# Kernel optimization log

Hardware: AMD Instinct MI355X
Metric: run time of the kernel (lower is better)

## Reference

```python
import jax, jax.numpy as jnp
import numpy as np

B, L, D_MODEL = 8, 2048, 768
D_INNER, D_STATE, DT_RANK, K = 1536, 16, 48, 4


def setup_inputs() -> dict:
    key = jax.random.key(0)
    ks = jax.random.split(key, 9)
    s = 0.02
    return {
        "hidden_states": jax.random.normal(ks[0], (B, L, D_MODEL), jnp.float32),
        "W_in": jax.random.normal(ks[1], (D_MODEL, 2 * D_INNER), jnp.float32) * s,
        "conv_w": jax.random.normal(ks[2], (D_INNER, 1, K), jnp.float32) * s,
        "conv_b": jax.random.normal(ks[3], (D_INNER,), jnp.float32) * s,
        "W_x": jax.random.normal(ks[4], (DT_RANK + 2 * D_STATE, D_INNER), jnp.float32) * s,
        "W_dt": jax.random.normal(ks[5], (D_INNER, DT_RANK), jnp.float32) * s,
        "b_dt": jax.random.normal(ks[6], (D_INNER,), jnp.float32) * s,
        "A_log": jax.random.normal(ks[7], (D_INNER, D_STATE), jnp.float32),
        "D_param": jax.random.normal(ks[8], (D_INNER,), jnp.float32),
    }


def _mamba(hidden_states, W_in, conv_w, conv_b, W_x, W_dt, b_dt, A_log, D_param):
    # in_proj then chunk into ssm branch (x) and gating residual (res)
    xz = hidden_states @ W_in                      # (B, L, 2*d_inner)
    x, res = jnp.split(xz, 2, axis=-1)             # each (B, L, d_inner)

    # causal depthwise conv over time, then SiLU
    xc = x.transpose(0, 2, 1)                      # (B, C, L)
    xc = jax.lax.conv_general_dilated(
        xc, conv_w, window_strides=(1,), padding=[(K - 1, 0)],
        feature_group_count=D_INNER, dimension_numbers=("NCH", "OIH", "NCH"))
    x = jax.nn.silu(xc + conv_b[None, :, None]).transpose(0, 2, 1)  # (B, L, d_inner)

    # input-dependent SSM parameters
    x_dbl = x @ W_x.T                              # (B, L, dt_rank + 2*d_state)
    dt = jax.nn.softplus(x_dbl[..., :DT_RANK] @ W_dt.T + b_dt)      # (B, L, d_inner)
    Bm = x_dbl[..., DT_RANK:DT_RANK + D_STATE]     # (B, L, d_state)
    Cm = x_dbl[..., DT_RANK + D_STATE:]            # (B, L, d_state)
    A = -jnp.exp(A_log)                            # (d_inner, d_state)

    def step(h, inp):
        x_t, dt_t, B_t, C_t = inp                  # (B,d_inner),(B,d_inner),(B,d_state),(B,d_state)
        dA = jnp.exp(dt_t[..., None] * A)          # (B, d_inner, d_state)
        dBx = (dt_t * x_t)[..., None] * B_t[:, None, :]
        h = dA * h + dBx
        y = jnp.einsum("bds,bs->bd", h, C_t)
        return h, y

    xs = (x.transpose(1, 0, 2), dt.transpose(1, 0, 2),
          Bm.transpose(1, 0, 2), Cm.transpose(1, 0, 2))
    h0 = jnp.zeros((x.shape[0], D_INNER, D_STATE), x.dtype)
    _, ys = jax.lax.scan(step, h0, xs)             # ys: (L, B, d_inner)
    y = ys.transpose(1, 0, 2) + x * D_param        # skip term
    return y * jax.nn.silu(res)                    # gated output (B, L, d_inner)


def reference(hidden_states, W_in, conv_w, conv_b, W_x, W_dt, b_dt, A_log, D_param):
    return _mamba(hidden_states, W_in, conv_w, conv_b, W_x, W_dt, b_dt, A_log, D_param)
```

## Files before the change

### kernel.cpp

```cpp
#include <hip/hip_runtime.h>
#include <hip/hip_bf16.h>
#include <stdint.h>

#define B_SZ 8
#define L_SZ 2048
#define DM 768
#define DI 1536
#define DS 16
#define DR 48
#define M_SZ (B_SZ * L_SZ)
#define N1 (2 * DI)

#define NC 64
#define TC (L_SZ / NC)
#define CH (B_SZ * DI)
#define KS 2
#define NT2 (DM / 32)
#define L2E 1.44269504088896f

typedef short short8 __attribute__((ext_vector_type(8)));
typedef float f32x4 __attribute__((ext_vector_type(4)));
typedef float f32x2 __attribute__((ext_vector_type(2)));

__device__ __forceinline__ ushort f2b(float f) {
  __hip_bfloat16 h = __float2bfloat16(f);
  return *reinterpret_cast<ushort*>(&h);
}
__device__ __forceinline__ float b2f(ushort u) {
  __hip_bfloat16 h;
  *reinterpret_cast<ushort*>(&h) = u;
  return __bfloat162float(h);
}
__device__ __forceinline__ ushort f2h(float f) {
  _Float16 h = (_Float16)f;
  return *reinterpret_cast<ushort*>(&h);
}
__device__ __forceinline__ float h2f(ushort u) {
  _Float16 h;
  *reinterpret_cast<ushort*>(&h) = u;
  return (float)h;
}

__device__ __forceinline__ void gl16(const ushort* g, ushort* l) {
  __builtin_amdgcn_global_load_lds(
      (const __attribute__((address_space(1))) void*)g,
      (__attribute__((address_space(3))) void*)l, 16, 0, 0);
}


__global__ __launch_bounds__(256) void prep_all(const float4* __restrict__ hs4,
                                                const float* __restrict__ w_in,
                                                const float* __restrict__ wx_f,
                                                const float* __restrict__ wdt_f,
                                                ushort4* __restrict__ A1,
                                                ushort* __restrict__ wt,
                                                ushort* __restrict__ wx_b,
                                                ushort* __restrict__ wdt_p) {
  const int n4 = M_SZ * DM / 4;
  const int nT = 3072 * 96;
  const int nwx = 80 * DI;
  const int nwdt = DI * 64;
  int idx = blockIdx.x * 256 + threadIdx.x;
  if (idx < n4) {
    float4 v = hs4[idx];
    ushort4 o;
    o.x = f2b(v.x); o.y = f2b(v.y); o.z = f2b(v.z); o.w = f2b(v.w);
    A1[idx] = o;
  } else if (idx < n4 + nT) {
    int j = idx - n4;
    int n = j % 3072;
    int kb = (j / 3072) * 8;
    short8 o;
#pragma unroll
    for (int q = 0; q < 8; ++q) o[q] = (short)f2b(w_in[(size_t)(kb + q) * 3072 + n]);
    *(short8*)(wt + (size_t)n * DM + kb) = o;
  } else if (idx < n4 + nT + nwx) {
    int j = idx - n4 - nT;
    wx_b[j] = f2b(wx_f[j]);
  } else if (idx < n4 + nT + nwx + nwdt) {
    int j = idx - n4 - nT - nwx;
    int col = j >> 6, k = j & 63;
    wdt_p[j] = (k < DR) ? f2b(wdt_f[col * DR + k]) : (ushort)0;
  }
}


__global__ __launch_bounds__(512, 1) void gemm_xz(const ushort* __restrict__ A,
                                                  const ushort* __restrict__ Bt,
                                                  ushort* __restrict__ xout,
                                                  ushort* __restrict__ gateout) {
  __shared__ ushort lds[49152];

  const int t = threadIdx.x;
  const int lane = t & 63;
  const int wid = t >> 6;
  const int wm = wid >> 2, wn = wid & 3;
  const int r = lane & 15, hi = lane >> 4;

  const int g = blockIdx.x;
  const int xcd = g & 7;
  const int local = g >> 3;
  const int bx = xcd * 8 + local / 12;
  const int by = local % 12;
  const int bm = bx * 256;
  const int bn = by * 256;

  const ushort* gsrc[4];
  int ldso[4];
#pragma unroll
  for (int i = 0; i < 4; ++i) {
    int c = wid * 4 + i;
    if (c < 16)
      gsrc[i] = A + (size_t)(bm + c * 16 + r) * DM + hi * 8;
    else
      gsrc[i] = Bt + (size_t)(bn + (c - 16) * 16 + r) * DM + hi * 8;
    ldso[i] = c * 512;
  }

  f32x4 acc[8][4];
#pragma unroll
  for (int m = 0; m < 8; ++m)
#pragma unroll
    for (int n = 0; n < 4; ++n) acc[m][n] = f32x4{0.f, 0.f, 0.f, 0.f};

  ushort* b0 = lds;
  ushort* b1 = lds + 16384;
  ushort* b2 = lds + 32768;

#pragma unroll
  for (int i = 0; i < 4; ++i) gl16(gsrc[i], b0 + ldso[i]);
#pragma unroll
  for (int i = 0; i < 4; ++i) gl16(gsrc[i] + 32, b1 + ldso[i]);
  asm volatile("s_waitcnt vmcnt(4)" ::: "memory");
  __builtin_amdgcn_s_barrier();

  for (int kt = 0; kt < NT2; ++kt) {
    const bool stage = (kt + 2 < NT2);
    const int koff = (kt + 2) * 32;

    short8 bfr[4];
#pragma unroll
    for (int n = 0; n < 4; ++n)
      bfr[n] = *(const short8*)&b0[(16 + wn * 4 + n) * 512 + lane * 8];

#pragma unroll
    for (int q = 0; q < 2; ++q) {
      short8 afr[4];
#pragma unroll
      for (int m = 0; m < 4; ++m)
        afr[m] = *(const short8*)&b0[(wm * 8 + q * 4 + m) * 512 + lane * 8];

      if (stage) {
        gl16(gsrc[2 * q] + koff, b2 + ldso[2 * q]);
        gl16(gsrc[2 * q + 1] + koff, b2 + ldso[2 * q + 1]);
      }

      asm volatile("s_barrier" ::: "memory");

      __builtin_amdgcn_s_setprio(1);
#pragma unroll
      for (int m = 0; m < 4; ++m)
#pragma unroll
        for (int n = 0; n < 4; ++n)
          acc[q * 4 + m][n] =
              __builtin_amdgcn_mfma_f32_16x16x32_bf16(afr[m], bfr[n], acc[q * 4 + m][n], 0, 0, 0);
      __builtin_amdgcn_s_setprio(0);

      if (q == 1) {
        if (stage)
          asm volatile("s_waitcnt vmcnt(4)" ::: "memory");
        else
          asm volatile("s_waitcnt vmcnt(0)" ::: "memory");
      }
      asm volatile("s_barrier" ::: "memory");
    }

    ushort* tmp = b0; b0 = b1; b1 = b2; b2 = tmp;
  }

  const bool isx = (bn < DI);
  ushort* outp = isx ? xout : gateout;
  const int cbase = bn - (isx ? 0 : DI) + wn * 64;
#pragma unroll
  for (int mf = 0; mf < 8; ++mf)
#pragma unroll
    for (int nf = 0; nf < 4; ++nf) {
      int col = cbase + nf * 16 + r;
#pragma unroll
      for (int j = 0; j < 4; ++j) {
        int row = bm + wm * 128 + mf * 16 + hi * 4 + j;
        float v = acc[mf][nf][j];
        if (!isx) v = v / (1.f + __expf(-v));
        outp[(size_t)row * DI + col] = f2b(v);
      }
    }
}


__global__ __launch_bounds__(256) void xdbl_conv(const ushort* __restrict__ xp,
                                                 const float* __restrict__ cw,
                                                 const float* __restrict__ cb,
                                                 const ushort* __restrict__ wx,
                                                 ushort* __restrict__ xc,
                                                 float* __restrict__ xdp) {
  __shared__ ushort Af[32 * 544];

  const int tid = threadIdx.x;
  const int row0 = blockIdx.x * 64;
  const int ks = blockIdx.y;

  const int lane = tid & 63, wid = tid >> 6;
  const int r = lane & 15, hi = lane >> 4;
  const int row0w = row0 + wid * 16;

  f32x4 acc[5];
#pragma unroll
  for (int n = 0; n < 5; ++n) acc[n] = f32x4{0.f, 0.f, 0.f, 0.f};

  const int rg = tid >> 5;
  const int c8 = tid & 31;
  const int col_loc = c8 * 8;
  const int chunkc = col_loc >> 5;
  const int hi_w = (col_loc & 31) >> 3;

  for (int sl = 0; sl < 3; ++sl) {
    const int kbeg = ks * 768 + sl * 256;
    if (sl) __syncthreads();

    {
      const int col = kbeg + col_loc;
      float4 cwv[8];
      float cbv[8];
#pragma unroll
      for (int e = 0; e < 8; ++e) {
        cwv[e] = *(const float4*)(cw + (size_t)(col + e) * 4);
        cbv[e] = cb[col + e];
      }
      short8 z8 = {0, 0, 0, 0, 0, 0, 0, 0};
#pragma unroll
      for (int j = 0; j < 8; ++j) {
        int row = row0 + rg * 8 + j;
        int l = row & (L_SZ - 1);
        const ushort* base = xp + (size_t)row * DI + col;
        short8 x0 = *(const short8*)base;
        short8 xm1 = (l >= 1) ? *(const short8*)(base - DI) : z8;
        short8 xm2 = (l >= 2) ? *(const short8*)(base - 2 * DI) : z8;
        short8 xm3 = (l >= 3) ? *(const short8*)(base - 3 * DI) : z8;
        short8 o;
#pragma unroll
        for (int e = 0; e < 8; ++e) {
          float4 w = cwv[e];
          float a = cbv[e] + w.x * b2f((ushort)xm3[e]) + w.y * b2f((ushort)xm2[e]) +
                    w.z * b2f((ushort)xm1[e]) + w.w * b2f((ushort)x0[e]);
          o[e] = (short)f2b(a / (1.f + __expf(-a)));
        }
        *(short8*)(xc + (size_t)row * DI + col) = o;
        int row_loc = rg * 8 + j;
        int chunk = (row_loc >> 4) * 8 + chunkc;
        int lane_t = (hi_w << 4) | (row_loc & 15);
        int slot = lane_t ^ (chunk & 7);
        *(short8*)&Af[chunk * 544 + slot * 8] = o;
      }
    }
    __syncthreads();

#pragma unroll
    for (int k0 = 0; k0 < 8; ++k0) {
      int chunk = wid * 8 + k0;
      short8 a = *(const short8*)&Af[chunk * 544 + ((lane ^ (chunk & 7)) * 8)];
      const int kk = kbeg + k0 * 32;
#pragma unroll
      for (int n = 0; n < 5; ++n) {
        short8 b = *(const short8*)(wx + (size_t)(n * 16 + r) * DI + kk + hi * 8);
        acc[n] = __builtin_amdgcn_mfma_f32_16x16x32_bf16(a, b, acc[n], 0, 0, 0);
      }
    }
  }

  float* op = xdp + (size_t)ks * M_SZ * 80;
#pragma unroll
  for (int n = 0; n < 5; ++n)
#pragma unroll
    for (int j = 0; j < 4; ++j)
      op[(size_t)(row0w + hi * 4 + j) * 80 + n * 16 + r] = acc[n][j];
}


__device__ __forceinline__ short8 pack8f(const float* p) {
  short8 v;
#pragma unroll
  for (int i = 0; i < 8; ++i) v[i] = (short)f2b(p[i]);
  return v;
}

__global__ __launch_bounds__(256) void dt_gemm(const float* __restrict__ xdp,
                                               const ushort* __restrict__ wdtp,
                                               const float* __restrict__ bdt,
                                               ushort* __restrict__ dt) {
  int wave = blockIdx.x * 4 + (threadIdx.x >> 6);
  int lane = threadIdx.x & 63;
  int r = lane & 15, hi = lane >> 4;
  int row0 = wave * 16;

  const float* p0 = xdp + (size_t)(row0 + r) * 80 + hi * 8;
  const float* p1 = p0 + (size_t)M_SZ * 80;

  float atmp[8];
  float4 q0 = *(const float4*)p0, q1 = *(const float4*)(p0 + 4);
  float4 s0 = *(const float4*)p1, s1 = *(const float4*)(p1 + 4);
  atmp[0] = q0.x + s0.x; atmp[1] = q0.y + s0.y; atmp[2] = q0.z + s0.z; atmp[3] = q0.w + s0.w;
  atmp[4] = q1.x + s1.x; atmp[5] = q1.y + s1.y; atmp[6] = q1.z + s1.z; atmp[7] = q1.w + s1.w;
  short8 a0 = pack8f(atmp);
  short8 a1 = {0, 0, 0, 0, 0, 0, 0, 0};
  if (hi < 2) {
    const float* p0b = p0 + 32 - hi * 8 + hi * 8;
    const float* q0p = xdp + (size_t)(row0 + r) * 80 + 32 + hi * 8;
    const float* q1p = q0p + (size_t)M_SZ * 80;
    float4 u0 = *(const float4*)q0p, u1 = *(const float4*)(q0p + 4);
    float4 v0 = *(const float4*)q1p, v1 = *(const float4*)(q1p + 4);
    atmp[0] = u0.x + v0.x; atmp[1] = u0.y + v0.y; atmp[2] = u0.z + v0.z; atmp[3] = u0.w + v0.w;
    atmp[4] = u1.x + v1.x; atmp[5] = u1.y + v1.y; atmp[6] = u1.z + v1.z; atmp[7] = u1.w + v1.w;
    a1 = pack8f(atmp);
    (void)p0b;
  }

  for (int nb = blockIdx.y * 6; nb < blockIdx.y * 6 + 6; ++nb) {
    int c0 = nb * 64;
    f32x4 acc[4];
#pragma unroll
    for (int n = 0; n < 4; ++n) acc[n] = f32x4{0.f, 0.f, 0.f, 0.f};
#pragma unroll
    for (int n = 0; n < 4; ++n) {
      const ushort* wp = wdtp + (size_t)(c0 + n * 16 + r) * 64;
      short8 b0 = *(const short8*)(wp + hi * 8);
      short8 b1 = *(const short8*)(wp + 32 + hi * 8);
      acc[n] = __builtin_amdgcn_mfma_f32_16x16x32_bf16(a0, b0, acc[n], 0, 0, 0);
      acc[n] = __builtin_amdgcn_mfma_f32_16x16x32_bf16(a1, b1, acc[n], 0, 0, 0);
    }
#pragma unroll
    for (int n = 0; n < 4; ++n)
#pragma unroll
      for (int j = 0; j < 4; ++j) {
        int col = c0 + n * 16 + r;
        float z = acc[n][j] + bdt[col];
        float sp = (z > 20.f) ? z : __logf(1.f + __expf(z));
        dt[(size_t)(row0 + hi * 4 + j) * DI + col] = f2h(sp);
      }
  }
}


__global__ __launch_bounds__(256) void scan_pass1(const ushort* __restrict__ dt,
                                                  const ushort* __restrict__ xc,
                                                  const float* __restrict__ xdp,
                                                  const float* __restrict__ A_log,
                                                  float* __restrict__ hend,
                                                  float* __restrict__ sumdt) {
  const int d = blockIdx.x * 256 + threadIdx.x;
  const int c = blockIdx.y, b = blockIdx.z;
  const int t0 = c * TC;

  __shared__ float Bs[TC * 16];
  for (int i = threadIdx.x; i < TC * 16; i += 256) {
    int tt = i >> 4, s = i & 15;
    size_t row = ((size_t)(b * L_SZ + t0 + tt)) * 80 + DR + s;
    Bs[i] = xdp[row] + xdp[(size_t)M_SZ * 80 + row];
  }

  f32x2 a2[8];
  const float4* al4 = (const float4*)(A_log + (size_t)d * DS);
#pragma unroll
  for (int q = 0; q < 4; ++q) {
    float4 v = al4[q];
    a2[2 * q] = f32x2{-__expf(v.x) * L2E, -__expf(v.y) * L2E};
    a2[2 * q + 1] = f32x2{-__expf(v.z) * L2E, -__expf(v.w) * L2E};
  }

  __syncthreads();

  f32x2 h2[8];
#pragma unroll
  for (int q = 0; q < 8; ++q) h2[q] = f32x2{0.f, 0.f};
  float sd = 0.f;

  const ushort* dtp = dt + ((size_t)b * L_SZ + t0) * DI + d;
  const ushort* xp = xc + ((size_t)b * L_SZ + t0) * DI + d;

  ushort dt0 = dtp[0], dt1 = dtp[DI];
  ushort xu0 = xp[0], xu1 = xp[DI];
  dtp += 2 * (size_t)DI; xp += 2 * (size_t)DI;
  const f32x4* bp4 = (const f32x4*)Bs;
#pragma unroll 2
  for (int tt = 0; tt < TC; ++tt) {
    ushort dtu = dt0, xu = xu0;
    dt0 = dt1; xu0 = xu1;
    dt1 = *dtp; xu1 = *xp;
    dtp += DI; xp += DI;
    float dtv = h2f(dtu);
    float xv = b2f(xu);
    sd += dtv;
    float dx = dtv * xv;
    f32x2 dts = f32x2{dtv, dtv};
    f32x2 dxs = f32x2{dx, dx};
#pragma unroll
    for (int q4 = 0; q4 < 4; ++q4) {
      f32x4 bq = bp4[q4];
#pragma unroll
      for (int hq = 0; hq < 2; ++hq) {
        int q = q4 * 2 + hq;
        f32x2 bv = f32x2{bq[2 * hq], bq[2 * hq + 1]};
        f32x2 arg, t2;
        asm("v_pk_mul_f32 %0, %1, %2" : "=v"(arg) : "v"(dts), "v"(a2[q]));
        float e0, e1;
        asm("v_exp_f32 %0, %1" : "=v"(e0) : "v"(arg[0]));
        asm("v_exp_f32 %0, %1" : "=v"(e1) : "v"(arg[1]));
        asm("v_pk_mul_f32 %0, %1, %2" : "=v"(t2) : "v"(dxs), "v"(bv));
        h2[q][0] = __builtin_fmaf(e0, h2[q][0], t2[0]);
        h2[q][1] = __builtin_fmaf(e1, h2[q][1], t2[1]);
      }
    }
    bp4 += 4;
  }

  const size_t ch = (size_t)b * DI + d;
  sumdt[ch * NC + c] = sd;
  f32x2* hp = (f32x2*)&hend[((size_t)c * CH + ch) * 16];
#pragma unroll
  for (int q = 0; q < 8; ++q) hp[q] = h2[q];
}


__global__ __launch_bounds__(256) void scan_pass2(const float* __restrict__ A_log,
                                                  const float* __restrict__ sumdt,
                                                  float* __restrict__ hbuf) {
  int idx = blockIdx.x * 256 + threadIdx.x;
  int ch = idx >> 4, s = idx & 15;
  int d = ch % DI;
  float A = -__expf(A_log[d * DS + s]);
  float h = 0.f;
  for (int c = 0; c < NC; ++c) {
    float* p = &hbuf[((size_t)c * CH + ch) * 16 + s];
    float he = *p;
    *p = h;
    float sd = sumdt[(size_t)ch * NC + c];
    h = __expf(A * sd) * h + he;
  }
}

__global__ __launch_bounds__(256) void scan_pass3(const ushort* __restrict__ dt,
                                                  const ushort* __restrict__ xc,
                                                  const float* __restrict__ xdp,
                                                  const ushort* __restrict__ gateb,
                                                  const float* __restrict__ A_log,
                                                  const float* __restrict__ Dp,
                                                  const float* __restrict__ hstart,
                                                  float* __restrict__ out) {
  const int d = blockIdx.x * 256 + threadIdx.x;
  const int c = blockIdx.y, b = blockIdx.z;
  const int t0 = c * TC;

  __shared__ float Bs[TC * 16];
  __shared__ float Cs[TC * 16];
  for (int i = threadIdx.x; i < TC * 16; i += 256) {
    int tt = i >> 4, s = i & 15;
    size_t row = ((size_t)(b * L_SZ + t0 + tt)) * 80;
    Bs[i] = xdp[row + DR + s] + xdp[(size_t)M_SZ * 80 + row + DR + s];
    Cs[i] = xdp[row + DR + DS + s] + xdp[(size_t)M_SZ * 80 + row + DR + DS + s];
  }

  f32x2 a2[8];
  const float4* al4 = (const float4*)(A_log + (size_t)d * DS);
#pragma unroll
  for (int q = 0; q < 4; ++q) {
    float4 v = al4[q];
    a2[2 * q] = f32x2{-__expf(v.x) * L2E, -__expf(v.y) * L2E};
    a2[2 * q + 1] = f32x2{-__expf(v.z) * L2E, -__expf(v.w) * L2E};
  }
  const float Dpv = Dp[d];

  const size_t ch = (size_t)b * DI + d;
  f32x2 h2[8];
  const f32x2* hp = (const f32x2*)&hstart[((size_t)c * CH + ch) * 16];
#pragma unroll
  for (int q = 0; q < 8; ++q) h2[q] = hp[q];

  __syncthreads();

  const ushort* dtp = dt + ((size_t)b * L_SZ + t0) * DI + d;
  const ushort* xp = xc + ((size_t)b * L_SZ + t0) * DI + d;
  const ushort* gp = gateb + ((size_t)b * L_SZ + t0) * DI + d;
  float* op = out + ((size_t)b * L_SZ + t0) * DI + d;

  ushort dt0 = dtp[0], dt1 = dtp[DI];
  ushort xu0 = xp[0], xu1 = xp[DI];
  ushort gu0 = gp[0], gu1 = gp[DI];
  dtp += 2 * (size_t)DI; xp += 2 * (size_t)DI; gp += 2 * (size_t)DI;
  const f32x4* bp4 = (const f32x4*)Bs;
  const f32x4* cp4 = (const f32x4*)Cs;
#pragma unroll 2
  for (int tt = 0; tt < TC; ++tt) {
    ushort dtu = dt0, xu = xu0, gu = gu0;
    dt0 = dt1; xu0 = xu1; gu0 = gu1;
    dt1 = *dtp; xu1 = *xp; gu1 = *gp;
    dtp += DI; xp += DI; gp += DI;
    float dtv = h2f(dtu);
    float xv = b2f(xu);
    float gv = b2f(gu);
    float dx = dtv * xv;
    f32x2 dts = f32x2{dtv, dtv};
    f32x2 dxs = f32x2{dx, dx};
    f32x2 ya = f32x2{0.f, 0.f}, yb = f32x2{0.f, 0.f};
#pragma unroll
    for (int q4 = 0; q4 < 4; ++q4) {
      f32x4 bq = bp4[q4];
      f32x4 cq = cp4[q4];
#pragma unroll
      for (int hq = 0; hq < 2; ++hq) {
        int q = q4 * 2 + hq;
        f32x2 bv = f32x2{bq[2 * hq], bq[2 * hq + 1]};
        f32x2 cv = f32x2{cq[2 * hq], cq[2 * hq + 1]};
        f32x2 arg, t2;
        asm("v_pk_mul_f32 %0, %1, %2" : "=v"(arg) : "v"(dts), "v"(a2[q]));
        float e0, e1;
        asm("v_exp_f32 %0, %1" : "=v"(e0) : "v"(arg[0]));
        asm("v_exp_f32 %0, %1" : "=v"(e1) : "v"(arg[1]));
        asm("v_pk_mul_f32 %0, %1, %2" : "=v"(t2) : "v"(dxs), "v"(bv));
        h2[q][0] = __builtin_fmaf(e0, h2[q][0], t2[0]);
        h2[q][1] = __builtin_fmaf(e1, h2[q][1], t2[1]);
        if (hq)
          asm("v_pk_fma_f32 %0, %1, %2, %0" : "+v"(yb) : "v"(h2[q]), "v"(cv));
        else
          asm("v_pk_fma_f32 %0, %1, %2, %0" : "+v"(ya) : "v"(h2[q]), "v"(cv));
      }
    }
    bp4 += 4; cp4 += 4;
    float y = (ya[0] + ya[1]) + (yb[0] + yb[1]);
    op[0] = (y + xv * Dpv) * gv;
    op += DI;
  }
}


extern "C" void kernel_launch(void* const* d_in, const int* in_sizes, int n_in,
                              void* d_out, int out_size, void* d_ws, size_t ws_size,
                              hipStream_t stream) {
  const float* hs     = (const float*)d_in[0];
  const float* W_in   = (const float*)d_in[1];
  const float* conv_w = (const float*)d_in[2];
  const float* conv_b = (const float*)d_in[3];
  const float* W_x    = (const float*)d_in[4];
  const float* W_dt   = (const float*)d_in[5];
  const float* b_dt   = (const float*)d_in[6];
  const float* A_log  = (const float*)d_in[7];
  const float* D_par  = (const float*)d_in[8];
  float* out = (float*)d_out;
  char* ws = (char*)d_ws;

  size_t o = 0;
  ushort* A1   = (ushort*)(ws + o); o += (size_t)M_SZ * DM * 2;
  ushort* Wt1  = (ushort*)(ws + o); o += (size_t)N1 * DM * 2;
  ushort* xpre = (ushort*)(ws + o); o += (size_t)M_SZ * DI * 2;
  ushort* gate = (ushort*)(ws + o); o += (size_t)M_SZ * DI * 2;
  ushort* xcv  = (ushort*)(ws + o); o += (size_t)M_SZ * DI * 2;
  ushort* dtb  = (ushort*)(ws + o); o += (size_t)M_SZ * DI * 2;
  float*  xdp  = (float*)(ws + o);  o += (size_t)KS * M_SZ * 80 * 4;
  ushort* Wxb  = (ushort*)(ws + o); o += (size_t)80 * DI * 2;
  ushort* Wdtp = (ushort*)(ws + o); o += (size_t)DI * 64 * 2;
  if (ws_size < o) return;

  float* hbuf  = (float*)(ws + 0);
  float* sumdt = (float*)(ws + (size_t)NC * CH * 16 * 4);

  const int nprep = M_SZ * DM / 4 + 3072 * 96 + 80 * DI + DI * 64;
  prep_all<<<dim3((nprep + 255) / 256), dim3(256), 0, stream>>>(
      (const float4*)hs, W_in, W_x, W_dt, (ushort4*)A1, Wt1, Wxb, Wdtp);

  gemm_xz<<<dim3((M_SZ / 256) * (N1 / 256)), dim3(512), 0, stream>>>(A1, Wt1, xpre, gate);

  xdbl_conv<<<dim3(M_SZ / 64, KS), dim3(256), 0, stream>>>(xpre, conv_w, conv_b, Wxb,
                                                           xcv, xdp);

  dt_gemm<<<dim3(M_SZ / 64, 4), dim3(256), 0, stream>>>(xdp, Wdtp, b_dt, dtb);

  scan_pass1<<<dim3(DI / 256, NC, B_SZ), dim3(256), 0, stream>>>(dtb, xcv, xdp, A_log, hbuf, sumdt);
  scan_pass2<<<dim3(CH * 16 / 256), dim3(256), 0, stream>>>(A_log, sumdt, hbuf);
  scan_pass3<<<dim3(DI / 256, NC, B_SZ), dim3(256), 0, stream>>>(dtb, xcv, xdp, gate,
                                                                 A_log, D_par, hbuf, out);
}
```

Baseline: 359.7 us.

## Software-pipeline LDS fragment loads across k-iterations in in_proj GEMM

```diff
diff --git a/kernel.cpp b/kernel.cpp
--- a/kernel.cpp
+++ b/kernel.cpp
@@ -134,48 +134,63 @@
   asm volatile("s_waitcnt vmcnt(4)" ::: "memory");
   __builtin_amdgcn_s_barrier();
 
+  short8 bfr[4], afr0[4], afr1[4], bfr_n[4], afr0_n[4];
+#pragma unroll
+  for (int n = 0; n < 4; ++n)
+    bfr[n] = *(const short8*)&b0[(16 + wn * 4 + n) * 512 + lane * 8];
+#pragma unroll
+  for (int m = 0; m < 4; ++m)
+    afr0[m] = *(const short8*)&b0[(wm * 8 + m) * 512 + lane * 8];
+
   for (int kt = 0; kt < NT2; ++kt) {
     const bool stage = (kt + 2 < NT2);
+    const bool more = (kt + 1 < NT2);
     const int koff = (kt + 2) * 32;
 
-    short8 bfr[4];
-#pragma unroll
-    for (int n = 0; n < 4; ++n)
-      bfr[n] = *(const short8*)&b0[(16 + wn * 4 + n) * 512 + lane * 8];
-
-#pragma unroll
-    for (int q = 0; q < 2; ++q) {
-      short8 afr[4];
+    if (stage) {
+#pragma unroll
+      for (int i = 0; i < 4; ++i) gl16(gsrc[i] + koff, b2 + ldso[i]);
+    }
+#pragma unroll
+    for (int m = 0; m < 4; ++m)
+      afr1[m] = *(const short8*)&b0[(wm * 8 + 4 + m) * 512 + lane * 8];
+
+    __builtin_amdgcn_s_setprio(1);
+#pragma unroll
+    for (int m = 0; m < 4; ++m)
+#pragma unroll
+      for (int n = 0; n < 4; ++n)
+        acc[m][n] = __builtin_amdgcn_mfma_f32_16x16x32_bf16(afr0[m], bfr[n], acc[m][n], 0, 0, 0);
+    __builtin_amdgcn_s_setprio(0);
+
+    if (stage)
+      asm volatile("s_waitcnt vmcnt(4)" ::: "memory");
+    else
+      asm volatile("s_waitcnt vmcnt(0)" ::: "memory");
+    asm volatile("s_waitcnt lgkmcnt(0)" ::: "memory");
+    asm volatile("s_barrier" ::: "memory");
+
+    if (more) {
+#pragma unroll
+      for (int n = 0; n < 4; ++n)
+        bfr_n[n] = *(const short8*)&b1[(16 + wn * 4 + n) * 512 + lane * 8];
 #pragma unroll
       for (int m = 0; m < 4; ++m)
-        afr[m] = *(const short8*)&b0[(wm * 8 + q * 4 + m) * 512 + lane * 8];
-
-      if (stage) {
-        gl16(gsrc[2 * q] + koff, b2 + ldso[2 * q]);
-        gl16(gsrc[2 * q + 1] + koff, b2 + ldso[2 * q + 1]);
-      }
-
-      asm volatile("s_barrier" ::: "memory");
-
-      __builtin_amdgcn_s_setprio(1);
-#pragma unroll
-      for (int m = 0; m < 4; ++m)
-#pragma unroll
-        for (int n = 0; n < 4; ++n)
-          acc[q * 4 + m][n] =
-              __builtin_amdgcn_mfma_f32_16x16x32_bf16(afr[m], bfr[n], acc[q * 4 + m][n], 0, 0, 0);
-      __builtin_amdgcn_s_setprio(0);
-
-      if (q == 1) {
-        if (stage)
-          asm volatile("s_waitcnt vmcnt(4)" ::: "memory");
-        else
-          asm volatile("s_waitcnt vmcnt(0)" ::: "memory");
-      }
-      asm volatile("s_barrier" ::: "memory");
-    }
+        afr0_n[m] = *(const short8*)&b1[(wm * 8 + m) * 512 + lane * 8];
+    }
+
+    __builtin_amdgcn_s_setprio(1);
+#pragma unroll
+    for (int m = 0; m < 4; ++m)
+#pragma unroll
+      for (int n = 0; n < 4; ++n)
+        acc[4 + m][n] =
+            __builtin_amdgcn_mfma_f32_16x16x32_bf16(afr1[m], bfr[n], acc[4 + m][n], 0, 0, 0);
+    __builtin_amdgcn_s_setprio(0);
 
     ushort* tmp = b0; b0 = b1; b1 = b2; b2 = tmp;
+#pragma unroll
+    for (int i = 0; i < 4; ++i) { bfr[i] = bfr_n[i]; afr0[i] = afr0_n[i]; }
   }
 
   const bool isx = (bn < DI);
@@ -313,7 +328,6 @@
   short8 a0 = pack8f(atmp);
   short8 a1 = {0, 0, 0, 0, 0, 0, 0, 0};
   if (hi < 2) {
-    const float* p0b = p0 + 32 - hi * 8 + hi * 8;
     const float* q0p = xdp + (size_t)(row0 + r) * 80 + 32 + hi * 8;
     const float* q1p = q0p + (size_t)M_SZ * 80;
     float4 u0 = *(const float4*)q0p, u1 = *(const float4*)(q0p + 4);
@@ -321,7 +335,6 @@
     atmp[0] = u0.x + v0.x; atmp[1] = u0.y + v0.y; atmp[2] = u0.z + v0.z; atmp[3] = u0.w + v0.w;
     atmp[4] = u1.x + v1.x; atmp[5] = u1.y + v1.y; atmp[6] = u1.z + v1.z; atmp[7] = u1.w + v1.w;
     a1 = pack8f(atmp);
-    (void)p0b;
   }
 
   for (int nb = blockIdx.y * 6; nb < blockIdx.y * 6 + 6; ++nb) {
```

Result: no change. 361.3 us (+0.4%).
